# Kernel tuning notes

Hardware: AMD Instinct MI355X
Metric: run time of the kernel (lower is better)

The kernel has to match this reference:

```python
import jax, jax.numpy as jnp
import numpy as np

B, S, D = 4, 2048, 1024
H, HD = 16, 64  # num_heads, head_dim
TD = H * HD     # total_dim
SCALE = HD ** -0.5


def setup_inputs() -> dict:
    key = jax.random.key(0)
    ks = jax.random.split(key, 9)
    std = 1.0 / np.sqrt(D)
    return {
        "x": jax.random.normal(ks[0], (B, S, D), dtype=jnp.float32),
        "Wq": jax.random.uniform(ks[1], (D, TD), jnp.float32, -std, std),
        "bq": jax.random.uniform(ks[2], (TD,), jnp.float32, -std, std),
        "Wk": jax.random.uniform(ks[3], (D, TD), jnp.float32, -std, std),
        "bk": jax.random.uniform(ks[4], (TD,), jnp.float32, -std, std),
        "Wv": jax.random.uniform(ks[5], (D, TD), jnp.float32, -std, std),
        "bv": jax.random.uniform(ks[6], (TD,), jnp.float32, -std, std),
        "Wo": jax.random.uniform(ks[7], (TD, D), jnp.float32, -std, std),
        "bo": jax.random.uniform(ks[8], (D,), jnp.float32, -std, std),
    }


def reference(x, Wq, bq, Wk, bk, Wv, bv, Wo, bo):
    # projections -> [B, H, S, HD]
    def split_heads(t):
        return t.reshape(B, S, H, HD).transpose(0, 2, 1, 3)

    q = split_heads(x @ Wq + bq)
    k = split_heads(x @ Wk + bk)
    v = split_heads(x @ Wv + bv)

    # attention scores [B, H, S, S]
    scores = jnp.einsum("bhqd,bhkd->bhqk", q, k) * SCALE
    weights = jax.nn.softmax(scores, axis=-1)
    # dropout is identity in eval mode (p effectively 0)
    attn = jnp.einsum("bhqk,bhkd->bhqd", weights, v)  # [B, H, S, HD]
    attn = attn.transpose(0, 2, 1, 3).reshape(B, S, TD)
    return attn @ Wo + bo
```

## Files before the change

kernel.cpp:

```cpp
#include <hip/hip_runtime.h>
#include <hip/hip_bf16.h>
#include <stdint.h>

#define B_ 4
#define S_ 2048
#define D_ 1024
#define H_ 16
#define HD_ 64
#define TD_ 1024

typedef __attribute__((ext_vector_type(4))) float f32x4;
typedef __attribute__((ext_vector_type(8))) __bf16 bf16x8;
typedef __attribute__((ext_vector_type(4))) __bf16 bf16x4;

__device__ __forceinline__ f32x4 mfma_16x16x32(bf16x8 a, bf16x8 b, f32x4 c) {
  return __builtin_amdgcn_mfma_f32_16x16x32_bf16(a, b, c, 0, 0, 0);
}

__device__ __forceinline__ float fexp2(float x) {
#if __has_builtin(__builtin_amdgcn_exp2f)
  return __builtin_amdgcn_exp2f(x);
#else
  return exp2f(x);
#endif
}

__device__ __forceinline__ uint32_t pkbf16(float lo, float hi) {
  uint32_t r;
  asm("v_cvt_pk_bf16_f32 %0, %1, %2" : "=v"(r) : "v"(lo), "v"(hi));
  return r;
}

__device__ __forceinline__ void gload16(const void* g, void* l) {
  __builtin_amdgcn_global_load_lds(
      (const __attribute__((address_space(1))) uint32_t*)(uintptr_t)g,
      (__attribute__((address_space(3))) uint32_t*)(uintptr_t)l,
      16, 0, 0);
}

__device__ __forceinline__ int xcd_swz(int flat, int nwg) {
  return (flat & 7) * (nwg >> 3) + (flat >> 3);
}


__global__ __launch_bounds__(256) void conv_x_kernel(const float* __restrict__ in,
                                                     __bf16* __restrict__ out) {
  size_t i = ((size_t)blockIdx.x * 256 + threadIdx.x) * 8;
  float4 a = *(const float4*)(in + i);
  float4 b = *(const float4*)(in + i + 4);
  bf16x8 o;
  o[0] = (__bf16)a.x; o[1] = (__bf16)a.y; o[2] = (__bf16)a.z; o[3] = (__bf16)a.w;
  o[4] = (__bf16)b.x; o[5] = (__bf16)b.y; o[6] = (__bf16)b.z; o[7] = (__bf16)b.w;
  *(bf16x8*)(out + i) = o;
}

__global__ __launch_bounds__(256) void wconv4_kernel(
    const float* __restrict__ w0, const float* __restrict__ w1,
    const float* __restrict__ w2, const float* __restrict__ w3,
    __bf16* __restrict__ o0, __bf16* __restrict__ o1,
    __bf16* __restrict__ o2, __bf16* __restrict__ o3, float scale0) {
  const float* in; __bf16* out; float scale;
  switch (blockIdx.z) {
    case 0: in = w0; out = o0; scale = scale0; break;
    case 1: in = w1; out = o1; scale = 1.0f; break;
    case 2: in = w2; out = o2; scale = 1.0f; break;
    default: in = w3; out = o3; scale = 1.0f; break;
  }
  __shared__ float t[64][65];
  const int bx = blockIdx.x * 64;
  const int by = blockIdx.y * 64;
  for (int e = threadIdx.x; e < 4096; e += 256) {
    int r = e >> 6, c = e & 63;
    t[r][c] = in[(size_t)(by + r) * 1024 + bx + c];
  }
  __syncthreads();
  for (int e = threadIdx.x; e < 4096; e += 256) {
    int r = e >> 6, c = e & 63;
    out[(size_t)(bx + r) * 1024 + by + c] = (__bf16)(t[c][r] * scale);
  }
}


#define STG_HALF(SLOT, KOFF)                                            \
  gload16(srcA + (KOFF), dstA + (SLOT) * 8192);                         \
  gload16(srcB + (KOFF), dstB + (SLOT) * 16384);                        \
  gload16(srcB + 131072 + (KOFF), dstB + (SLOT) * 16384 + 8192);

#define COMPUTE_HALF(SLOT)                                              \
  {                                                                     \
    bf16x8 afr[4], bb[4];                                               \
    _Pragma("unroll") for (int mi = 0; mi < 4; ++mi)                    \
      afr[mi] = *(const bf16x8*)(aptr + (SLOT) * 8192 + mi * 1024);     \
    _Pragma("unroll") for (int ni = 0; ni < 4; ++ni)                    \
      bb[ni] = *(const bf16x8*)(bptr + (SLOT) * 16384 + ni * 1024);     \
    __builtin_amdgcn_s_setprio(1);                                      \
    _Pragma("unroll") for (int mi = 0; mi < 4; ++mi)                    \
      _Pragma("unroll") for (int ni = 0; ni < 4; ++ni)                  \
        acc[mi][ni] = mfma_16x16x32(afr[mi], bb[ni], acc[mi][ni]);      \
    __builtin_amdgcn_s_setprio(0);                                      \
  }

#define BAR_LGKM  asm volatile("s_waitcnt lgkmcnt(0)\n\ts_barrier" ::: "memory")
#define BAR_VM(N) asm volatile("s_waitcnt vmcnt(" #N ")\n\ts_barrier" ::: "memory")

template <int MODE, int NT>
__global__ __launch_bounds__(512, 4) void gemm256(
    const __bf16* __restrict__ A, const __bf16* __restrict__ Bt,
    const float* __restrict__ b0, const float* __restrict__ b1,
    const float* __restrict__ b2, void* __restrict__ o0,
    void* __restrict__ o1, void* __restrict__ o2, float qscale) {
  __shared__ char SM[49152];
  const int tid = threadIdx.x, lane = tid & 63, wid = tid >> 6;
  const int lrow = lane & 15, g = lane >> 4;
  const int wm = wid >> 2, wn = wid & 3;
  const int flat = blockIdx.y * NT + blockIdx.x;
  const int swz = xcd_swz(flat, 64 * NT);
  const int n0 = (swz % NT) * 256, m0 = (swz / NT) * 128;

  f32x4 acc[4][4];
  const f32x4 zero = {0.f, 0.f, 0.f, 0.f};
#pragma unroll
  for (int i = 0; i < 4; ++i)
#pragma unroll
    for (int j = 0; j < 4; ++j) acc[i][j] = zero;

  const int r0 = tid >> 2, c0 = tid & 3;
  const int csw = c0 ^ ((r0 >> 1) & 3);
  const __bf16* srcA = A + (size_t)(m0 + r0) * 1024 + csw * 8;
  const __bf16* srcB = Bt + (size_t)(n0 + r0) * 1024 + csw * 8;
  char* dstA = SM + wid * 1024;
  char* dstB = SM + 16384 + wid * 1024;

  const int sw = (lrow >> 1) & 3;
  const char* aptr = SM + (wm * 64 + lrow) * 64 + ((g ^ sw) << 4);
  const char* bptr = SM + 16384 + (wn * 64 + lrow) * 64 + ((g ^ sw) << 4);

  STG_HALF(0, 0)
  STG_HALF(1, 32)
  srcA += 64; srcB += 64;
  BAR_VM(3);

  for (int it = 0; it < 15; ++it) {
    COMPUTE_HALF(0)
    BAR_LGKM;
    STG_HALF(0, 0)
    BAR_VM(3);
    COMPUTE_HALF(1)
    BAR_LGKM;
    STG_HALF(1, 32)
    BAR_VM(3);
    srcA += 64; srcB += 64;
  }
  COMPUTE_HALF(0)
  BAR_LGKM;
  BAR_VM(0);
  COMPUTE_HALF(1)

  if constexpr (MODE == 0) {
    const int sel = n0 >> 10;
    if (sel < 2) {
      const float* bias = sel ? b1 : b0;
      const float bsc = sel ? 1.0f : qscale;
      __bf16* Out = (__bf16*)(sel ? o1 : o0);
#pragma unroll
      for (int mi = 0; mi < 4; ++mi) {
#pragma unroll
        for (int ni = 0; ni < 4; ++ni) {
          const int mbase = m0 + wm * 64 + mi * 16 + g * 4;
          const int nloc = (n0 & 1023) + wn * 64 + ni * 16 + lrow;
          const float bvc = bias[nloc] * bsc;
          const int h = nloc >> 6, hd = nloc & 63;
#pragma unroll
          for (int r = 0; r < 4; ++r) {
            const int m = mbase + r;
            const int b = m >> 11, s = m & 2047;
            Out[((size_t)(b * H_ + h) * S_ + s) * HD_ + hd] = (__bf16)(acc[mi][ni][r] + bvc);
          }
        }
      }
    } else {
      __bf16* Vout = (__bf16*)o2;
#pragma unroll
      for (int mi = 0; mi < 4; ++mi) {
#pragma unroll
        for (int ni = 0; ni < 4; ++ni) {
          const int mbase = m0 + wm * 64 + mi * 16 + g * 4;
          const int t = (n0 & 1023) + wn * 64 + ni * 16 + lrow;
          const float bvc = b2[t];
          bf16x4 w;
#pragma unroll
          for (int r = 0; r < 4; ++r) w[r] = (__bf16)(acc[mi][ni][r] + bvc);
          *(bf16x4*)(Vout + (size_t)t * (B_ * S_) + mbase) = w;
        }
      }
    }
  } else {
    float* Cout = (float*)o0;
#pragma unroll
    for (int mi = 0; mi < 4; ++mi) {
#pragma unroll
      for (int ni = 0; ni < 4; ++ni) {
        const int mbase = m0 + wm * 64 + mi * 16 + g * 4;
        const int ncol = n0 + wn * 64 + ni * 16 + lrow;
        const float bvc = b0[ncol];
#pragma unroll
        for (int r = 0; r < 4; ++r)
          Cout[(size_t)(mbase + r) * (NT * 256) + ncol] = acc[mi][ni][r] + bvc;
      }
    }
  }
}


__global__ __launch_bounds__(512, 8) void attn_kernel(
    const __bf16* __restrict__ Q, const __bf16* __restrict__ Kp,
    const __bf16* __restrict__ VT, __bf16* __restrict__ O) {
  const int flat = blockIdx.y * gridDim.x + blockIdx.x;
  const int swz = (flat & 7) * 128 + (flat >> 3);
  const int bh = swz >> 4;
  const int q0 = (swz & 15) * 128;
  const int tid = threadIdx.x, lane = tid & 63, wid = tid >> 6;
  const int lrow = lane & 15, g = lane >> 4;
  const int s7 = lrow & 7;
  const int b = bh >> 4, h = bh & 15;

  const __bf16* Qb = Q + (size_t)bh * S_ * HD_;

  __shared__ char SMEM[32768];

  const int qrow = q0 + wid * 16 + lrow;
  const bf16x8 qf0 = *(const bf16x8*)(Qb + (size_t)qrow * HD_ + g * 8);
  const bf16x8 qf1 = *(const bf16x8*)(Qb + (size_t)qrow * HD_ + 32 + g * 8);

  bf16x8 ones;
#pragma unroll
  for (int i = 0; i < 8; ++i) ones[i] = (__bf16)1.0f;

  const int row0 = tid >> 3, sg0 = tid & 7;
  const int kc0 = sg0 ^ (row0 & 7);
  const int kvoff = row0 * HD_ + kc0 * 8;
  const int vvoff = row0 * (B_ * S_) + kc0 * 8;
  const __bf16* Kt = Kp + (size_t)bh * S_ * HD_;
  const __bf16* Vt = VT + (size_t)(h * HD_) * (B_ * S_) + b * S_;
  char* kd0 = SMEM + wid * 1024;
  char* vd0 = SMEM + 16384 + wid * 1024;

  const char* addrA = SMEM + lrow * 128 + ((g ^ s7) << 4);
  const char* addrB = SMEM + lrow * 128 + (((4 + g) ^ s7) << 4);

  f32x4 lacc;
  f32x4 oa[4];
  const f32x4 zero = {0.f, 0.f, 0.f, 0.f};
  const f32x4 minit = {-8.f, -8.f, -8.f, -8.f};
  lacc = zero;
#pragma unroll
  for (int i = 0; i < 4; ++i) oa[i] = zero;

  gload16(Kt + kvoff, kd0);
  gload16(Vt + vvoff, vd0);
  Kt += 64 * HD_; Vt += 64;
  __syncthreads();

  auto stage = [&](const int bo) {
    gload16(Kt + kvoff, kd0 + bo);
    gload16(Vt + vvoff, vd0 + bo);
    Kt += 64 * HD_; Vt += 64;
  };

  auto compute = [&](const int bo) {
    f32x4 sc[4];
    __builtin_amdgcn_s_setprio(1);
#pragma unroll
    for (int kt = 0; kt < 4; ++kt) {
      bf16x8 kf0 = *(const bf16x8*)(addrA + bo + kt * 2048);
      bf16x8 kf1 = *(const bf16x8*)(addrB + bo + kt * 2048);
      f32x4 c = minit;
      c = mfma_16x16x32(kf0, qf0, c);
      c = mfma_16x16x32(kf1, qf1, c);
      sc[kt] = c;
    }
    __builtin_amdgcn_s_setprio(0);

#pragma unroll
    for (int kt = 0; kt < 4; ++kt)
#pragma unroll
      for (int r = 0; r < 4; ++r) sc[kt][r] = fexp2(sc[kt][r]);

    bf16x8 pfrag[2];
#pragma unroll
    for (int s = 0; s < 2; ++s) {
      uint32_t a0 = pkbf16(sc[2 * s][0], sc[2 * s][1]);
      uint32_t a1 = pkbf16(sc[2 * s][2], sc[2 * s][3]);
      uint32_t b0 = pkbf16(sc[2 * s + 1][0], sc[2 * s + 1][1]);
      uint32_t b1 = pkbf16(sc[2 * s + 1][2], sc[2 * s + 1][3]);
      asm volatile("v_permlane32_swap_b32 %0, %1" : "+v"(a0), "+v"(b0));
      asm volatile("v_permlane32_swap_b32 %0, %1" : "+v"(a1), "+v"(b1));
      asm volatile("v_permlane16_swap_b32 %0, %1" : "+v"(a0), "+v"(b0));
      asm volatile("v_permlane16_swap_b32 %0, %1" : "+v"(a1), "+v"(b1));
      union { uint32_t u[4]; bf16x8 v; } pu;
      pu.u[0] = a0; pu.u[1] = a1; pu.u[2] = b0; pu.u[3] = b1;
      pfrag[s] = pu.v;
    }

    __builtin_amdgcn_s_setprio(1);
#pragma unroll
    for (int band = 0; band < 4; ++band) {
      bf16x8 vf0 = *(const bf16x8*)(addrA + 16384 + bo + band * 2048);
      bf16x8 vf1 = *(const bf16x8*)(addrB + 16384 + bo + band * 2048);
      oa[band] = mfma_16x16x32(vf0, pfrag[0], oa[band]);
      oa[band] = mfma_16x16x32(vf1, pfrag[1], oa[band]);
    }
    lacc = mfma_16x16x32(ones, pfrag[0], lacc);
    lacc = mfma_16x16x32(ones, pfrag[1], lacc);
    __builtin_amdgcn_s_setprio(0);
  };

  for (int t = 0; t < S_ / 64; t += 2) {
    stage(8192);
    compute(0);
    __syncthreads();
    if (t + 2 < S_ / 64) stage(0);
    compute(8192);
    __syncthreads();
  }

  const float inv = 1.f / lacc[0];
  __bf16* op = O + ((size_t)(b * S_ + qrow)) * TD_ + h * HD_;
#pragma unroll
  for (int band = 0; band < 4; ++band) {
    bf16x4 w;
#pragma unroll
    for (int r = 0; r < 4; ++r) w[r] = (__bf16)(oa[band][r] * inv);
    *(bf16x4*)(op + band * 16 + g * 4) = w;
  }
}


extern "C" void kernel_launch(void* const* d_in, const int* in_sizes, int n_in,
                              void* d_out, int out_size, void* d_ws, size_t ws_size,
                              hipStream_t stream) {
  const float* x = (const float*)d_in[0];
  const float* Wq = (const float*)d_in[1];
  const float* bq = (const float*)d_in[2];
  const float* Wk = (const float*)d_in[3];
  const float* bk = (const float*)d_in[4];
  const float* Wv = (const float*)d_in[5];
  const float* bv = (const float*)d_in[6];
  const float* Wo = (const float*)d_in[7];
  const float* bo = (const float*)d_in[8];

  char* p = (char*)d_ws;
  const size_t SZ_X = (size_t)B_ * S_ * D_ * 2;
  const size_t SZ_W = (size_t)D_ * TD_ * 2;
  const size_t SZ_QKV = (size_t)B_ * H_ * S_ * HD_ * 2;
  __bf16* xb = (__bf16*)p;  p += SZ_X;
  __bf16* wqT = (__bf16*)p; p += SZ_W;
  __bf16* wkT = (__bf16*)p; p += SZ_W;
  __bf16* wvT = (__bf16*)p; p += SZ_W;
  __bf16* woT = (__bf16*)p; p += SZ_W;
  __bf16* Qb = (__bf16*)p;  p += SZ_QKV;
  __bf16* Kb = (__bf16*)p;  p += SZ_QKV;
  __bf16* VTb = (__bf16*)p; p += SZ_QKV;
  __bf16* attn = xb;

  const float SCALE_Q = 0.125f * 1.4426950408889634f;

  conv_x_kernel<<<4096, 256, 0, stream>>>(x, xb);
  wconv4_kernel<<<dim3(16, 16, 4), 256, 0, stream>>>(Wq, Wk, Wv, Wo,
                                                     wqT, wkT, wvT, woT, SCALE_Q);

  gemm256<0, 12><<<dim3(12, 64), 512, 0, stream>>>(
      xb, wqT, bq, bk, bv, Qb, Kb, VTb, SCALE_Q);

  attn_kernel<<<dim3(16, 64), 512, 0, stream>>>(Qb, Kb, VTb, attn);

  gemm256<1, 4><<<dim3(4, 64), 512, 0, stream>>>(
      attn, woT, bo, nullptr, nullptr, d_out, nullptr, nullptr, 1.0f);
}
```

Baseline: 179.0 us.

## Replace output projection GEMM with 128x128-tile double-buffered ring kernel

The output projection previously used the 256-wide gemm256 template with 256 blocks, which underfills the GPU's CUs. A dedicated 128x128-tile kernel with 4 waves launches 512 blocks and uses a two-slot LDS ring, loading the next K slice while computing the current one. This aims to raise occupancy and overlap global loads with MFMA work. In exchange, smaller tiles mean less data reuse per block and more total global traffic.

```diff
diff --git a/kernel.cpp b/kernel.cpp
--- a/kernel.cpp
+++ b/kernel.cpp
@@ -212,6 +212,91 @@
 }
 
 
+#define STG_O(SLOT, KOFF)                                               \
+  gload16(srcA + (KOFF), dstA + (SLOT) * 8192);                         \
+  gload16(srcA + 65536 + (KOFF), dstA + (SLOT) * 8192 + 4096);          \
+  gload16(srcB + (KOFF), dstB + (SLOT) * 8192);                         \
+  gload16(srcB + 65536 + (KOFF), dstB + (SLOT) * 8192 + 4096);
+
+#define COMPUTE_O(SLOT)                                                 \
+  {                                                                     \
+    bf16x8 afr[4], bb[4];                                               \
+    _Pragma("unroll") for (int mi = 0; mi < 4; ++mi)                    \
+      afr[mi] = *(const bf16x8*)(aptr + (SLOT) * 8192 + mi * 1024);     \
+    _Pragma("unroll") for (int ni = 0; ni < 4; ++ni)                    \
+      bb[ni] = *(const bf16x8*)(bptr + (SLOT) * 8192 + ni * 1024);      \
+    __builtin_amdgcn_s_setprio(1);                                      \
+    _Pragma("unroll") for (int mi = 0; mi < 4; ++mi)                    \
+      _Pragma("unroll") for (int ni = 0; ni < 4; ++ni)                  \
+        acc[mi][ni] = mfma_16x16x32(afr[mi], bb[ni], acc[mi][ni]);      \
+    __builtin_amdgcn_s_setprio(0);                                      \
+  }
+
+__global__ __launch_bounds__(256, 4) void gemm_out_ring(
+    const __bf16* __restrict__ A, const __bf16* __restrict__ Bt,
+    const float* __restrict__ bias, float* __restrict__ Cout) {
+  __shared__ char SM[32768];
+  const int tid = threadIdx.x, lane = tid & 63, wid = tid >> 6;
+  const int lrow = lane & 15, g = lane >> 4;
+  const int wm = wid >> 1, wn = wid & 1;
+  const int flat = blockIdx.y * 8 + blockIdx.x;
+  const int swz = xcd_swz(flat, 512);
+  const int n0 = (swz & 7) * 128, m0 = (swz >> 3) * 128;
+
+  f32x4 acc[4][4];
+  const f32x4 zero = {0.f, 0.f, 0.f, 0.f};
+#pragma unroll
+  for (int i = 0; i < 4; ++i)
+#pragma unroll
+    for (int j = 0; j < 4; ++j) acc[i][j] = zero;
+
+  const int r0 = tid >> 2, c0 = tid & 3;
+  const int csw = c0 ^ ((r0 >> 1) & 3);
+  const __bf16* srcA = A + (size_t)(m0 + r0) * 1024 + csw * 8;
+  const __bf16* srcB = Bt + (size_t)(n0 + r0) * 1024 + csw * 8;
+  char* dstA = SM + wid * 1024;
+  char* dstB = SM + 16384 + wid * 1024;
+
+  const int sw = (lrow >> 1) & 3;
+  const char* aptr = SM + (wm * 64 + lrow) * 64 + ((g ^ sw) << 4);
+  const char* bptr = SM + 16384 + (wn * 64 + lrow) * 64 + ((g ^ sw) << 4);
+
+  STG_O(0, 0)
+  STG_O(1, 32)
+  srcA += 64; srcB += 64;
+  BAR_VM(4);
+
+  for (int it = 0; it < 15; ++it) {
+    COMPUTE_O(0)
+    BAR_LGKM;
+    STG_O(0, 0)
+    BAR_VM(4);
+    COMPUTE_O(1)
+    BAR_LGKM;
+    STG_O(1, 32)
+    BAR_VM(4);
+    srcA += 64; srcB += 64;
+  }
+  COMPUTE_O(0)
+  BAR_LGKM;
+  BAR_VM(0);
+  COMPUTE_O(1)
+
+#pragma unroll
+  for (int mi = 0; mi < 4; ++mi) {
+#pragma unroll
+    for (int ni = 0; ni < 4; ++ni) {
+      const int mbase = m0 + wm * 64 + mi * 16 + g * 4;
+      const int ncol = n0 + wn * 64 + ni * 16 + lrow;
+      const float bvc = bias[ncol];
+#pragma unroll
+      for (int r = 0; r < 4; ++r)
+        Cout[(size_t)(mbase + r) * 1024 + ncol] = acc[mi][ni][r] + bvc;
+    }
+  }
+}
+
+
 __global__ __launch_bounds__(512, 8) void attn_kernel(
     const __bf16* __restrict__ Q, const __bf16* __restrict__ Kp,
     const __bf16* __restrict__ VT, __bf16* __restrict__ O) {
@@ -374,6 +459,5 @@
 
   attn_kernel<<<dim3(16, 64), 512, 0, stream>>>(Qb, Kb, VTb, attn);
 
-  gemm256<1, 4><<<dim3(4, 64), 512, 0, stream>>>(
-      attn, woT, bo, nullptr, nullptr, d_out, nullptr, nullptr, 1.0f);
-}
+  gemm_out_ring<<<dim3(8, 64), 256, 0, stream>>>(attn, woT, bo, (float*)d_out);
+}
```

Result: no change. 178.1 us (-0.5%).
